# Performance work log

Hardware: AMD Instinct MI355X
Metric: run time of the kernel (lower is better)

## Reference

```python
import jax, jax.numpy as jnp
import numpy as np

H = W = 2048


def _grad(x, kernel):
    # torch F.conv2d(x, kernel, stride=1, padding=1); kernel [2,1,2,1] (OIHW)
    # output: [N, 2, H+1, W+2]
    y = jax.lax.conv_general_dilated(
        x, kernel, window_strides=(1, 1), padding=[(1, 1), (1, 1)],
        dimension_numbers=("NCHW", "OIHW", "NCHW"))
    return jnp.abs(y)


def _grayscale(r3):
    # emulates to_pil_image (mul 255 -> uint8) + PIL 'L' conversion + to_tensor (/255)
    # PIL: L = (R*19595 + G*38470 + B*7471 + 0x8000) >> 16
    q = jnp.floor(jnp.clip(r3, 0.0, 1.0) * 255.0)
    gs = jnp.floor((q[0] * 19595.0 + q[1] * 38470.0 + q[2] * 7471.0 + 32768.0) / 65536.0) / 255.0
    # PIL round-trip breaks autograd in the original -> detached here too
    return jax.lax.stop_gradient(gs)[None, None]  # [1,1,H,W]


def _histeq(im, nbins=256):
    # numpy: histogram(density=True) -> cumsum -> /cdf[-1] -> interp(x, bins[:-1], cdf)
    flat = im.reshape(-1)
    hist, edges = jnp.histogram(flat, bins=nbins, density=True)
    cdf = jnp.cumsum(hist)
    cdf = cdf / cdf[-1]
    return jnp.interp(flat, edges[:-1], cdf).reshape(im.shape)


def setup_inputs() -> dict:
    key = jax.random.key(0)
    k1, k2, k3 = jax.random.split(key, 3)
    return {
        "input_im": jax.random.uniform(k1, (1, 3, H, W), dtype=jnp.float32),
        "R": jax.random.uniform(k2, (1, 3, H, W), dtype=jnp.float32),
        "L": jax.random.uniform(k3, (1, 1, H, W), dtype=jnp.float32),
    }


def reference(input_im, R, L):
    kx = jnp.array([0.0, 0.0, -1.0, 1.0], dtype=jnp.float32).reshape(2, 1, 2, 1)
    ky = jnp.transpose(kx, (2, 1, 0, 3))  # torch permute(2,1,0,3)

    # histogram-equalized target (detached in original via .detach().cpu().numpy())
    im_max = jnp.max(input_im, axis=1, keepdims=True)           # [1,1,H,W]
    im_eq = jax.lax.stop_gradient(_histeq(im_max[0]))[None]     # [1,1,H,W]

    # recon_loss_low
    L3 = jnp.concatenate([L, L, L], axis=1)
    recon_low = jnp.mean(jnp.abs(R * L3 - input_im))

    # recon_loss_low_eq
    R_max = jnp.max(R, axis=1, keepdims=True)
    recon_low_eq = jnp.mean(jnp.abs(R_max - im_eq))

    # R_low_loss_smooth (grayscale is detached)
    Rg = _grayscale(R[0])                  # [1,1,H,W]
    a = _grad(Rg, kx)                      # [1,2,H+1,W+2]
    b = _grad(Rg, ky)
    r_smooth = jnp.mean(a + b)             # torch.abs of already-abs values

    # Ismooth_loss_low: smooth(L, R)
    ismooth = jnp.mean(_grad(L, kx) * jnp.exp(-10.0 * a)
                       + _grad(L, ky) * jnp.exp(-10.0 * b))

    return recon_low + 0.1 * ismooth + 0.1 * recon_low_eq + 0.01 * r_smooth
```

## Files before the change

### kernel.cpp

```cpp
#include <hip/hip_runtime.h>
#include <stdint.h>

#define HH 2048
#define WW 2048
#define HW (HH * WW)
#define N4 (HW / 4)
#define FB 512
#define G1 512
#define G3 512


__device__ __forceinline__ float gray_pil(float r, float g, float b) {
    float qr = floorf(fminf(fmaxf(r, 0.f), 1.f) * 255.f);
    float qg = floorf(fminf(fmaxf(g, 0.f), 1.f) * 255.f);
    float qb = floorf(fminf(fmaxf(b, 0.f), 1.f) * 255.f);
    float s = floorf((qr * 19595.f + qg * 38470.f + qb * 7471.f + 32768.f) * (1.f / 65536.f));
    return s * (1.f / 255.f);
}

__global__ __launch_bounds__(1024, 4) void hist_k(const float* __restrict__ im, uint32_t* __restrict__ ctl) {
    __shared__ uint32_t lh[FB];
    int t = threadIdx.x;
    if (t < FB) lh[t] = 0u;
    __syncthreads();

    const float4* im4 = (const float4*)im;
    int tid = blockIdx.x * 1024 + t;
#pragma unroll
    for (int k = 0; k < 2; ++k) {
        int i = tid + k * (G1 * 1024);
        float4 a = im4[i], b = im4[i + N4], c = im4[i + 2 * N4];
        float m[4];
        m[0] = fmaxf(a.x, fmaxf(b.x, c.x));
        m[1] = fmaxf(a.y, fmaxf(b.y, c.y));
        m[2] = fmaxf(a.z, fmaxf(b.z, c.z));
        m[3] = fmaxf(a.w, fmaxf(b.w, c.w));
#pragma unroll
        for (int j = 0; j < 4; ++j) {
            int bin = (int)(m[j] * (float)FB);
            bin = bin < 0 ? 0 : (bin > FB - 1 ? FB - 1 : bin);
            atomicAdd(&lh[bin], 1u);
        }
    }
    __syncthreads();
    if (t < FB && lh[t]) atomicAdd(&ctl[t], lh[t]);
}

__global__ __launch_bounds__(256) void cdf_k(uint32_t* __restrict__ ctl) {
    __shared__ uint32_t sf[FB];
    __shared__ uint32_t sc[256];
    __shared__ uint32_t smm[2];
    int t = threadIdx.x;
    sf[t] = ctl[t];
    sf[t + 256] = ctl[t + 256];
    sc[t] = 0u;
    if (t == 0) { smm[0] = FB; smm[1] = 0u; }
    __syncthreads();
    if (sf[t]) { atomicMin(&smm[0], (uint32_t)t); atomicMax(&smm[1], (uint32_t)t); }
    if (sf[t + 256]) { atomicMin(&smm[0], (uint32_t)(t + 256)); atomicMax(&smm[1], (uint32_t)(t + 256)); }
    __syncthreads();
    float gmin = (float)smm[0] * (1.0f / (float)FB);
    float gmax = (float)(smm[1] + 1u) * (1.0f / (float)FB);
    float inv_dw = 256.0f / (gmax - gmin);
#pragma unroll
    for (int jj = 0; jj < 2; ++jj) {
        int j = t + jj * 256;
        uint32_t cnt = sf[j];
        if (cnt) {
            float c = ((float)j + 0.5f) * (1.0f / (float)FB);
            int q = (int)((c - gmin) * inv_dw);
            q = q < 0 ? 0 : (q > 255 ? 255 : q);
            atomicAdd(&sc[q], cnt);
        }
    }
    __syncthreads();
#pragma unroll
    for (int d = 1; d < 256; d <<= 1) {
        uint32_t v = (t >= d) ? sc[t - d] : 0u;
        __syncthreads();
        sc[t] += v;
        __syncthreads();
    }
    float* cf = (float*)ctl;
    cf[t] = (float)((double)sc[t] * (1.0 / (double)HW));
    if (t == 0) { cf[256] = gmin; cf[257] = gmax; }
}

__device__ __forceinline__ void px(float r0, float r1, float r2,
                                   float i0, float i1, float i2, float l,
                                   float& rgp, float& lp,
                                   const float* __restrict__ scdf, float gmin, float inv_dw,
                                   float& a0, float& a1, float& a2,
                                   float& a3, float& a4, float& a5) {
    a0 += fabsf(r0 * l - i0) + fabsf(r1 * l - i1) + fabsf(r2 * l - i2);
    float rmax = fmaxf(r0, fmaxf(r1, r2));
    float imax = fmaxf(i0, fmaxf(i1, i2));
    float t = (imax - gmin) * inv_dw;
    t = fmaxf(t, 0.f);
    int bi = (int)t;
    float eq;
    if (bi >= 255) eq = scdf[255];
    else {
        float fr = t - (float)bi;
        eq = scdf[bi] + fr * (scdf[bi + 1] - scdf[bi]);
    }
    a1 += fabsf(rmax - eq);
    float rg = gray_pil(r0, r1, r2);
    a3 += rg;
    a5 += l * __expf(-10.f * rg);
    float drg = fabsf(rg - rgp);
    a2 += drg;
    a4 += fabsf(l - lp) * __expf(-10.f * drg);
    rgp = rg;
    lp = l;
}

__global__ __launch_bounds__(1024, 4)
void main_k(const float* __restrict__ im, const float* __restrict__ R,
            const float* __restrict__ L, uint32_t* __restrict__ ctl,
            float* __restrict__ out) {
    __shared__ float scdf[256];
    __shared__ float red[6][16];
    int t = threadIdx.x;

    const float* cf = (const float*)ctl;
    if (t < 256) scdf[t] = cf[t];
    float gmin = cf[256];
    float gmax = cf[257];
    float inv_dw = 256.0f / (gmax - gmin);
    __syncthreads();

    int w = (t & 511) * 4;
    int h0 = blockIdx.x * 4 + ((t >> 9) * 2);

    float a0 = 0.f, a1 = 0.f, a2 = 0.f, a3 = 0.f, a4 = 0.f, a5 = 0.f;
    float rgp[4], lp[4];
    if (h0 > 0) {
        int p = (h0 - 1) * WW + w;
        float4 Ra = *(const float4*)(R + p);
        float4 Rb = *(const float4*)(R + p + HW);
        float4 Rc = *(const float4*)(R + p + 2 * HW);
        float4 Lv = *(const float4*)(L + p);
        rgp[0] = gray_pil(Ra.x, Rb.x, Rc.x); lp[0] = Lv.x;
        rgp[1] = gray_pil(Ra.y, Rb.y, Rc.y); lp[1] = Lv.y;
        rgp[2] = gray_pil(Ra.z, Rb.z, Rc.z); lp[2] = Lv.z;
        rgp[3] = gray_pil(Ra.w, Rb.w, Rc.w); lp[3] = Lv.w;
    } else {
        rgp[0] = rgp[1] = rgp[2] = rgp[3] = 0.f;
        lp[0] = lp[1] = lp[2] = lp[3] = 0.f;
    }

#pragma unroll
    for (int h = h0; h < h0 + 2; ++h) {
        int p = h * WW + w;
        float4 r0 = *(const float4*)(R + p);
        float4 r1 = *(const float4*)(R + p + HW);
        float4 r2 = *(const float4*)(R + p + 2 * HW);
        float4 i0 = *(const float4*)(im + p);
        float4 i1 = *(const float4*)(im + p + HW);
        float4 i2 = *(const float4*)(im + p + 2 * HW);
        float4 lv = *(const float4*)(L + p);
        px(r0.x, r1.x, r2.x, i0.x, i1.x, i2.x, lv.x, rgp[0], lp[0], scdf, gmin, inv_dw, a0, a1, a2, a3, a4, a5);
        px(r0.y, r1.y, r2.y, i0.y, i1.y, i2.y, lv.y, rgp[1], lp[1], scdf, gmin, inv_dw, a0, a1, a2, a3, a4, a5);
        px(r0.z, r1.z, r2.z, i0.z, i1.z, i2.z, lv.z, rgp[2], lp[2], scdf, gmin, inv_dw, a0, a1, a2, a3, a4, a5);
        px(r0.w, r1.w, r2.w, i0.w, i1.w, i2.w, lv.w, rgp[3], lp[3], scdf, gmin, inv_dw, a0, a1, a2, a3, a4, a5);
    }
    if (h0 + 2 == HH) {
#pragma unroll
        for (int j = 0; j < 4; ++j) {
            a2 += rgp[j];
            a4 += lp[j] * __expf(-10.f * rgp[j]);
        }
    }

    for (int off = 32; off; off >>= 1) {
        a0 += __shfl_down(a0, off);
        a1 += __shfl_down(a1, off);
        a2 += __shfl_down(a2, off);
        a3 += __shfl_down(a3, off);
        a4 += __shfl_down(a4, off);
        a5 += __shfl_down(a5, off);
    }
    int lane = t & 63, wv = t >> 6;
    if (lane == 0) {
        red[0][wv] = a0; red[1][wv] = a1; red[2][wv] = a2;
        red[3][wv] = a3; red[4][wv] = a4; red[5][wv] = a5;
    }
    __syncthreads();
    if (t == 0) {
        float s0 = 0, s1 = 0, s2 = 0, s3 = 0, s4 = 0, s5 = 0;
        for (int k = 0; k < 16; k++) {
            s0 += red[0][k]; s1 += red[1][k]; s2 += red[2][k];
            s3 += red[3][k]; s4 += red[4][k]; s5 += red[5][k];
        }
        float* acc = (float*)(ctl + 512);
        atomicAdd(&acc[0], s0);
        atomicAdd(&acc[1], s1);
        atomicAdd(&acc[2], s2);
        atomicAdd(&acc[3], s3);
        atomicAdd(&acc[4], s4);
        atomicAdd(&acc[5], s5);
        __threadfence();
        uint32_t old = atomicAdd(&ctl[518], 1u);
        if (old == G3 - 1) {
            float v0 = atomicAdd(&acc[0], 0.f);
            float v1 = atomicAdd(&acc[1], 0.f);
            float v2 = atomicAdd(&acc[2], 0.f);
            float v3 = atomicAdd(&acc[3], 0.f);
            float v4 = atomicAdd(&acc[4], 0.f);
            float v5 = atomicAdd(&acc[5], 0.f);
            float recon_low = v0 / (3.0f * (float)HW);
            float recon_eq = v1 / (float)HW;
            float denom = 2.0f * 2049.0f * 2050.0f;
            float r_smooth = (v2 + 2.f * v3) / denom;
            float ismooth = (v4 + 2.f * v5) / denom;
            out[0] = recon_low + 0.1f * ismooth + 0.1f * recon_eq + 0.01f * r_smooth;
        }
    }
}

extern "C" void kernel_launch(void* const* d_in, const int* in_sizes, int n_in,
                              void* d_out, int out_size, void* d_ws, size_t ws_size,
                              hipStream_t stream) {
    const float* im = (const float*)d_in[0];
    const float* R = (const float*)d_in[1];
    const float* L = (const float*)d_in[2];
    float* out = (float*)d_out;
    uint32_t* ctl = (uint32_t*)d_ws;

    hipMemsetAsync(d_ws, 0, 519 * 4, stream);
    hipLaunchKernelGGL(hist_k, dim3(G1), dim3(1024), 0, stream, im, ctl);
    hipLaunchKernelGGL(cdf_k, dim3(1), dim3(256), 0, stream, ctl);
    hipLaunchKernelGGL(main_k, dim3(G3), dim3(1024), 0, stream, im, R, L, ctl, out);
}
```

Baseline: 197.1 us.

## Fuse CDF into histogram last block, double per-thread work, use per-block partials

Folds the single-block CDF kernel into the histogram kernel: the last block to finish, found through an atomic counter, builds the CDF, which removes one launch. Each thread now handles four float4 groups in both kernels, with all loads issued up front, and the grid sizes are halved. In main_k each thread processes four rows instead of two. Block sums go to a per-block partial buffer that the last block reduces, replacing contended float atomics. This adds workspace-size dependence and relies on the shared counter at ctl[518] spanning both kernels.

```diff
diff --git a/kernel.cpp b/kernel.cpp
--- a/kernel.cpp
+++ b/kernel.cpp
@@ -6,8 +6,9 @@
 #define HW (HH * WW)
 #define N4 (HW / 4)
 #define FB 512
-#define G1 512
-#define G3 512
+#define G1H 256
+#define G3M 256
+#define STRIDE (G1H * 1024)
 
 
 __device__ __forceinline__ float gray_pil(float r, float g, float b) {
@@ -18,71 +19,74 @@
     return s * (1.f / 255.f);
 }
 
-__global__ __launch_bounds__(1024, 4) void hist_k(const float* __restrict__ im, uint32_t* __restrict__ ctl) {
+__global__ __launch_bounds__(1024, 4)
+void hist_k(const float* __restrict__ im, uint32_t* __restrict__ ctl) {
     __shared__ uint32_t lh[FB];
+    __shared__ uint32_t sc[256];
+    __shared__ uint32_t smm[2];
+    __shared__ uint32_t lastf;
     int t = threadIdx.x;
     if (t < FB) lh[t] = 0u;
     __syncthreads();
 
     const float4* im4 = (const float4*)im;
     int tid = blockIdx.x * 1024 + t;
-#pragma unroll
-    for (int k = 0; k < 2; ++k) {
-        int i = tid + k * (G1 * 1024);
-        float4 a = im4[i], b = im4[i + N4], c = im4[i + 2 * N4];
-        float m[4];
-        m[0] = fmaxf(a.x, fmaxf(b.x, c.x));
-        m[1] = fmaxf(a.y, fmaxf(b.y, c.y));
-        m[2] = fmaxf(a.z, fmaxf(b.z, c.z));
-        m[3] = fmaxf(a.w, fmaxf(b.w, c.w));
-#pragma unroll
-        for (int j = 0; j < 4; ++j) {
-            int bin = (int)(m[j] * (float)FB);
-            bin = bin < 0 ? 0 : (bin > FB - 1 ? FB - 1 : bin);
-            atomicAdd(&lh[bin], 1u);
-        }
-    }
+    float4 A0 = im4[tid],              B0 = im4[tid + N4],              C0 = im4[tid + 2 * N4];
+    float4 A1 = im4[tid + STRIDE],     B1 = im4[tid + STRIDE + N4],     C1 = im4[tid + STRIDE + 2 * N4];
+    float4 A2 = im4[tid + 2 * STRIDE], B2 = im4[tid + 2 * STRIDE + N4], C2 = im4[tid + 2 * STRIDE + 2 * N4];
+    float4 A3 = im4[tid + 3 * STRIDE], B3 = im4[tid + 3 * STRIDE + N4], C3 = im4[tid + 3 * STRIDE + 2 * N4];
+
+#define HBIN(a, b, c) { \
+        float m0 = fmaxf(a.x, fmaxf(b.x, c.x)); \
+        float m1 = fmaxf(a.y, fmaxf(b.y, c.y)); \
+        float m2 = fmaxf(a.z, fmaxf(b.z, c.z)); \
+        float m3 = fmaxf(a.w, fmaxf(b.w, c.w)); \
+        int b0 = (int)(m0 * (float)FB); b0 = b0 < 0 ? 0 : (b0 > FB - 1 ? FB - 1 : b0); \
+        int b1 = (int)(m1 * (float)FB); b1 = b1 < 0 ? 0 : (b1 > FB - 1 ? FB - 1 : b1); \
+        int b2 = (int)(m2 * (float)FB); b2 = b2 < 0 ? 0 : (b2 > FB - 1 ? FB - 1 : b2); \
+        int b3 = (int)(m3 * (float)FB); b3 = b3 < 0 ? 0 : (b3 > FB - 1 ? FB - 1 : b3); \
+        atomicAdd(&lh[b0], 1u); atomicAdd(&lh[b1], 1u); \
+        atomicAdd(&lh[b2], 1u); atomicAdd(&lh[b3], 1u); }
+    HBIN(A0, B0, C0)
+    HBIN(A1, B1, C1)
+    HBIN(A2, B2, C2)
+    HBIN(A3, B3, C3)
+#undef HBIN
+
     __syncthreads();
     if (t < FB && lh[t]) atomicAdd(&ctl[t], lh[t]);
-}
-
-__global__ __launch_bounds__(256) void cdf_k(uint32_t* __restrict__ ctl) {
-    __shared__ uint32_t sf[FB];
-    __shared__ uint32_t sc[256];
-    __shared__ uint32_t smm[2];
-    int t = threadIdx.x;
-    sf[t] = ctl[t];
-    sf[t + 256] = ctl[t + 256];
-    sc[t] = 0u;
+    __syncthreads();
+    if (t == 0) {
+        __threadfence();
+        lastf = (atomicAdd(&ctl[518], 1u) == G1H - 1) ? 1u : 0u;
+    }
+    __syncthreads();
+    if (!lastf) return;
+
+    if (t < FB) lh[t] = atomicAdd(&ctl[t], 0u);
+    if (t < 256) sc[t] = 0u;
     if (t == 0) { smm[0] = FB; smm[1] = 0u; }
     __syncthreads();
-    if (sf[t]) { atomicMin(&smm[0], (uint32_t)t); atomicMax(&smm[1], (uint32_t)t); }
-    if (sf[t + 256]) { atomicMin(&smm[0], (uint32_t)(t + 256)); atomicMax(&smm[1], (uint32_t)(t + 256)); }
+    if (t < FB && lh[t]) { atomicMin(&smm[0], (uint32_t)t); atomicMax(&smm[1], (uint32_t)t); }
     __syncthreads();
     float gmin = (float)smm[0] * (1.0f / (float)FB);
     float gmax = (float)(smm[1] + 1u) * (1.0f / (float)FB);
     float inv_dw = 256.0f / (gmax - gmin);
-#pragma unroll
-    for (int jj = 0; jj < 2; ++jj) {
-        int j = t + jj * 256;
-        uint32_t cnt = sf[j];
-        if (cnt) {
-            float c = ((float)j + 0.5f) * (1.0f / (float)FB);
-            int q = (int)((c - gmin) * inv_dw);
-            q = q < 0 ? 0 : (q > 255 ? 255 : q);
-            atomicAdd(&sc[q], cnt);
-        }
-    }
-    __syncthreads();
-#pragma unroll
+    if (t < FB && lh[t]) {
+        float c = ((float)t + 0.5f) * (1.0f / (float)FB);
+        int q = (int)((c - gmin) * inv_dw);
+        q = q < 0 ? 0 : (q > 255 ? 255 : q);
+        atomicAdd(&sc[q], lh[t]);
+    }
+    __syncthreads();
     for (int d = 1; d < 256; d <<= 1) {
-        uint32_t v = (t >= d) ? sc[t - d] : 0u;
+        uint32_t v = (t < 256 && t >= d) ? sc[t - d] : 0u;
         __syncthreads();
-        sc[t] += v;
+        if (t < 256) sc[t] += v;
         __syncthreads();
     }
     float* cf = (float*)ctl;
-    cf[t] = (float)((double)sc[t] * (1.0 / (double)HW));
+    if (t < 256) cf[t] = (float)((double)sc[t] * (1.0 / (double)HW));
     if (t == 0) { cf[256] = gmin; cf[257] = gmax; }
 }
 
@@ -118,9 +122,11 @@
 __global__ __launch_bounds__(1024, 4)
 void main_k(const float* __restrict__ im, const float* __restrict__ R,
             const float* __restrict__ L, uint32_t* __restrict__ ctl,
+            float* __restrict__ part, int use_part,
             float* __restrict__ out) {
     __shared__ float scdf[256];
     __shared__ float red[6][16];
+    __shared__ uint32_t lastf;
     int t = threadIdx.x;
 
     const float* cf = (const float*)ctl;
@@ -130,8 +136,9 @@
     float inv_dw = 256.0f / (gmax - gmin);
     __syncthreads();
 
-    int w = (t & 511) * 4;
-    int h0 = blockIdx.x * 4 + ((t >> 9) * 2);
+    int tid = blockIdx.x * 1024 + t;
+    int w = (tid & 511) * 4;
+    int h0 = (tid >> 9) * 4;
 
     float a0 = 0.f, a1 = 0.f, a2 = 0.f, a3 = 0.f, a4 = 0.f, a5 = 0.f;
     float rgp[4], lp[4];
@@ -151,8 +158,8 @@
     }
 
 #pragma unroll
-    for (int h = h0; h < h0 + 2; ++h) {
-        int p = h * WW + w;
+    for (int hh = 0; hh < 4; ++hh) {
+        int p = (h0 + hh) * WW + w;
         float4 r0 = *(const float4*)(R + p);
         float4 r1 = *(const float4*)(R + p + HW);
         float4 r2 = *(const float4*)(R + p + 2 * HW);
@@ -165,7 +172,7 @@
         px(r0.z, r1.z, r2.z, i0.z, i1.z, i2.z, lv.z, rgp[2], lp[2], scdf, gmin, inv_dw, a0, a1, a2, a3, a4, a5);
         px(r0.w, r1.w, r2.w, i0.w, i1.w, i2.w, lv.w, rgp[3], lp[3], scdf, gmin, inv_dw, a0, a1, a2, a3, a4, a5);
     }
-    if (h0 + 2 == HH) {
+    if (h0 + 4 == HH) {
 #pragma unroll
         for (int j = 0; j < 4; ++j) {
             a2 += rgp[j];
@@ -193,16 +200,57 @@
             s0 += red[0][k]; s1 += red[1][k]; s2 += red[2][k];
             s3 += red[3][k]; s4 += red[4][k]; s5 += red[5][k];
         }
-        float* acc = (float*)(ctl + 512);
-        atomicAdd(&acc[0], s0);
-        atomicAdd(&acc[1], s1);
-        atomicAdd(&acc[2], s2);
-        atomicAdd(&acc[3], s3);
-        atomicAdd(&acc[4], s4);
-        atomicAdd(&acc[5], s5);
+        if (use_part) {
+            float* pp = part + blockIdx.x * 6;
+            atomicExch(&pp[0], s0); atomicExch(&pp[1], s1); atomicExch(&pp[2], s2);
+            atomicExch(&pp[3], s3); atomicExch(&pp[4], s4); atomicExch(&pp[5], s5);
+        } else {
+            float* acc = (float*)(ctl + 512);
+            atomicAdd(&acc[0], s0); atomicAdd(&acc[1], s1); atomicAdd(&acc[2], s2);
+            atomicAdd(&acc[3], s3); atomicAdd(&acc[4], s4); atomicAdd(&acc[5], s5);
+        }
         __threadfence();
-        uint32_t old = atomicAdd(&ctl[518], 1u);
-        if (old == G3 - 1) {
+        lastf = (atomicAdd(&ctl[518], 1u) == (uint32_t)(G1H + G3M - 1)) ? 1u : 0u;
+    }
+    __syncthreads();
+    if (!lastf) return;
+
+    if (use_part) {
+        float s0 = 0.f, s1 = 0.f, s2 = 0.f, s3 = 0.f, s4 = 0.f, s5 = 0.f;
+        if (t < G3M) {
+            float* pp = part + t * 6;
+            s0 = atomicAdd(&pp[0], 0.f); s1 = atomicAdd(&pp[1], 0.f); s2 = atomicAdd(&pp[2], 0.f);
+            s3 = atomicAdd(&pp[3], 0.f); s4 = atomicAdd(&pp[4], 0.f); s5 = atomicAdd(&pp[5], 0.f);
+        }
+        for (int off = 32; off; off >>= 1) {
+            s0 += __shfl_down(s0, off);
+            s1 += __shfl_down(s1, off);
+            s2 += __shfl_down(s2, off);
+            s3 += __shfl_down(s3, off);
+            s4 += __shfl_down(s4, off);
+            s5 += __shfl_down(s5, off);
+        }
+        if (lane == 0) {
+            red[0][wv] = s0; red[1][wv] = s1; red[2][wv] = s2;
+            red[3][wv] = s3; red[4][wv] = s4; red[5][wv] = s5;
+        }
+        __syncthreads();
+        if (t == 0) {
+            float v0 = 0, v1 = 0, v2 = 0, v3 = 0, v4 = 0, v5 = 0;
+            for (int k = 0; k < 16; k++) {
+                v0 += red[0][k]; v1 += red[1][k]; v2 += red[2][k];
+                v3 += red[3][k]; v4 += red[4][k]; v5 += red[5][k];
+            }
+            float recon_low = v0 / (3.0f * (float)HW);
+            float recon_eq = v1 / (float)HW;
+            float denom = 2.0f * 2049.0f * 2050.0f;
+            float r_smooth = (v2 + 2.f * v3) / denom;
+            float ismooth = (v4 + 2.f * v5) / denom;
+            out[0] = recon_low + 0.1f * ismooth + 0.1f * recon_eq + 0.01f * r_smooth;
+        }
+    } else {
+        if (t == 0) {
+            float* acc = (float*)(ctl + 512);
             float v0 = atomicAdd(&acc[0], 0.f);
             float v1 = atomicAdd(&acc[1], 0.f);
             float v2 = atomicAdd(&acc[2], 0.f);
@@ -228,8 +276,10 @@
     float* out = (float*)d_out;
     uint32_t* ctl = (uint32_t*)d_ws;
 
+    int use_part = (ws_size >= (size_t)((520 + 6 * G3M) * 4 + 32)) ? 1 : 0;
+    float* part = (float*)(ctl + 520);
+
     hipMemsetAsync(d_ws, 0, 519 * 4, stream);
-    hipLaunchKernelGGL(hist_k, dim3(G1), dim3(1024), 0, stream, im, ctl);
-    hipLaunchKernelGGL(cdf_k, dim3(1), dim3(256), 0, stream, ctl);
-    hipLaunchKernelGGL(main_k, dim3(G3), dim3(1024), 0, stream, im, R, L, ctl, out);
-}
+    hipLaunchKernelGGL(hist_k, dim3(G1H), dim3(1024), 0, stream, im, ctl);
+    hipLaunchKernelGGL(main_k, dim3(G3M), dim3(1024), 0, stream, im, R, L, ctl, part, use_part, out);
+}
```

Result: faster. 188.1 us (-4.5%).
